# Performance work log

Hardware: AMD Instinct MI355X
Metric: run time of the kernel (lower is better)

## Reference

```python
import jax, jax.numpy as jnp
import numpy as np

B, S, D, H = 32, 512, 512, 8  # note: source requires S == D due to swapped shape tuple in multi_head_attention
DK = D // H  # 64
FF = 200     # hard-coded FFN width in source
LN_EPS = 1e-5


def setup_inputs() -> dict:
    key = jax.random.key(0)
    ks = jax.random.split(key, 20)
    s = 0.02
    return {
        "x": jax.random.normal(ks[0], (B, S, D), dtype=jnp.float32),
        # per-head projections, stacked: torch Linear weight shape is [out, in] = [DK, D]
        "Wq": jax.random.normal(ks[1], (H, DK, D), dtype=jnp.float32) * s,
        "bq": jax.random.normal(ks[2], (H, DK), dtype=jnp.float32) * s,
        "Wk": jax.random.normal(ks[3], (H, DK, D), dtype=jnp.float32) * s,
        "bk": jax.random.normal(ks[4], (H, DK), dtype=jnp.float32) * s,
        "Wv": jax.random.normal(ks[5], (H, DK, D), dtype=jnp.float32) * s,
        "bv": jax.random.normal(ks[6], (H, DK), dtype=jnp.float32) * s,
        "Wo": jax.random.normal(ks[7], (D, D), dtype=jnp.float32) * s,
        "bo": jax.random.normal(ks[8], (D,), dtype=jnp.float32) * s,
        "W1": jax.random.normal(ks[9], (FF, D), dtype=jnp.float32) * s,
        "b1": jax.random.normal(ks[10], (FF,), dtype=jnp.float32) * s,
        "W2": jax.random.normal(ks[11], (FF, FF), dtype=jnp.float32) * s,
        "b2": jax.random.normal(ks[12], (FF,), dtype=jnp.float32) * s,
        "W3": jax.random.normal(ks[13], (D, FF), dtype=jnp.float32) * s,
        "b3": jax.random.normal(ks[14], (D,), dtype=jnp.float32) * s,
        # single SHARED LayerNorm over last two dims (S, D)
        "gamma": jnp.ones((S, D), dtype=jnp.float32),
        "beta": jnp.zeros((S, D), dtype=jnp.float32),
    }


def _layernorm2d(y, gamma, beta):
    # torch LayerNorm(normalized_shape=(S, D)): normalize over last two axes, biased variance
    m = jnp.mean(y, axis=(-2, -1), keepdims=True)
    v = jnp.mean(jnp.square(y - m), axis=(-2, -1), keepdims=True)
    return (y - m) * jax.lax.rsqrt(v + LN_EPS) * gamma + beta


def reference(x, Wq, bq, Wk, bk, Wv, bv, Wo, bo, W1, b1, W2, b2, W3, b3, gamma, beta):
    # --- multi-head attention (vectorized over the original per-head Python loop) ---
    q = jnp.einsum('bsd,hkd->bhsk', x, Wq) + bq[None, :, None, :]
    k = jnp.einsum('bsd,hkd->bhsk', x, Wk) + bk[None, :, None, :]
    v = jnp.einsum('bsd,hkd->bhsk', x, Wv) + bv[None, :, None, :]
    scores = jnp.einsum('bhsk,bhtk->bhst', q, k) / jnp.sqrt(jnp.float32(DK))
    attn = jax.nn.softmax(scores, axis=-1)
    heads = jnp.einsum('bhst,bhtk->bhsk', attn, v)          # [B,H,S,DK]
    concat = heads.transpose(0, 2, 1, 3).reshape(B, S, D)    # concat heads along feature dim
    y = jnp.einsum('bsd,ed->bse', concat, Wo) + bo + x       # output proj + residual
    # --- post-attention LayerNorm (shared params) ---
    y = _layernorm2d(y, gamma, beta)
    # --- feed-forward: D -> 200 -> 200 -> D, residual, LayerNorm (same shared LN) ---
    f = jax.nn.relu(jnp.einsum('bsd,fd->bsf', y, W1) + b1)
    f = jax.nn.relu(jnp.einsum('bsf,gf->bsg', f, W2) + b2)
    f = jnp.einsum('bsf,df->bsd', f, W3) + b3
    y = _layernorm2d(f + y, gamma, beta)
    # --- final LayerNorm (same shared LN again) ---
    return _layernorm2d(y, gamma, beta)
```

## Files before the change

### kernel.cpp

```cpp
#include <hip/hip_runtime.h>
#include <hip/hip_bf16.h>
#include <stdint.h>

#define B_  32
#define S_  512
#define D_  512
#define H_  8
#define DK_ 64
#define FF_ 200
#define FFP 256
#define M_  (B_*S_)
#define MSD ((size_t)B_*S_*D_)
#define NQKV 1536

typedef __hip_bfloat16 bf16;
typedef __attribute__((ext_vector_type(8))) short short8;
typedef __attribute__((ext_vector_type(4))) float f32x4;
typedef __attribute__((ext_vector_type(4))) unsigned short us4;

__device__ inline float b2f(bf16 v) { return __bfloat162float(v); }
__device__ inline bf16  f2b(float v){ return __float2bfloat16(v); }
__device__ inline unsigned short f2bu(float v) {
  union { bf16 h; unsigned short u; } cv; cv.h = __float2bfloat16(v); return cv.u;
}
__device__ inline float bu2f(unsigned short u) {
  union { unsigned short u; bf16 h; } cv; cv.u = u; return b2f(cv.h);
}
__device__ __forceinline__ void async16(const bf16* g, bf16* l) {
  __builtin_amdgcn_global_load_lds((const __attribute__((address_space(1))) void*)g,
                                   (__attribute__((address_space(3))) void*)l, 16, 0, 0);
}

__global__ void detect_kernel(const unsigned short* __restrict__ xu, int* __restrict__ flag,
                              float* __restrict__ stats) {
  __shared__ int mx[256];
  const int tid = threadIdx.x;
  if (tid < 192) stats[tid] = 0.f;
  int m = 0;
  for (int i = tid * 2; i < 8192; i += 512) {
    int e = (xu[i] >> 7) & 0xFF;
    m = m > e ? m : e;
  }
  mx[tid] = m;
  __syncthreads();
  for (int st = 128; st; st >>= 1) {
    if (tid < st) mx[tid] = mx[tid] > mx[tid + st] ? mx[tid] : mx[tid + st];
    __syncthreads();
  }
  if (tid == 0) *flag = (mx[0] >= 0xC0) ? 1 : 0;
}

__global__ __launch_bounds__(256) void cvt_x8(const void* __restrict__ in, bf16* __restrict__ out,
                                              const int* __restrict__ flag) {
  const bool f32in = (*flag != 0);
  size_t i = ((size_t)blockIdx.x * 256 + threadIdx.x) * 8;
  const size_t stride = (size_t)gridDim.x * 256 * 8;
  for (; i < MSD; i += stride) {
    if (f32in) {
      const float4 a = ((const float4*)in)[i/4];
      const float4 b = ((const float4*)in)[i/4 + 1];
      uint4 o; unsigned short* po = (unsigned short*)&o;
      po[0]=f2bu(a.x); po[1]=f2bu(a.y); po[2]=f2bu(a.z); po[3]=f2bu(a.w);
      po[4]=f2bu(b.x); po[5]=f2bu(b.y); po[6]=f2bu(b.z); po[7]=f2bu(b.w);
      *(uint4*)((unsigned short*)out + i) = o;
    } else {
      *(uint4*)((unsigned short*)out + i) = *(const uint4*)((const unsigned short*)in + i);
    }
  }
}

struct Seg { const void* src; void* dst; int srcRows, srcK, dstK, total; };
struct Segs { Seg s[16]; unsigned int isbf; };

__global__ __launch_bounds__(256) void cvt_all(Segs sg, const int* __restrict__ flag) {
  const bool f32in = (*flag != 0);
  const int seg = blockIdx.x & 15;
  const Seg sd = sg.s[seg];
  const int stride = (gridDim.x >> 4) * 256;
  const bool nopad = (sd.srcK == sd.dstK);
  for (int i = (blockIdx.x >> 4) * 256 + threadIdx.x; i < sd.total; i += stride) {
    int sidx; bool valid;
    if (nopad) { sidx = i; valid = (i < sd.srcRows * sd.srcK); }
    else {
      int r = i / sd.dstK, c = i - r * sd.dstK;
      valid = (r < sd.srcRows) && (c < sd.srcK);
      sidx = r * sd.srcK + c;
    }
    float v = 0.f;
    if (valid) v = f32in ? ((const float*)sd.src)[sidx] : b2f(((const bf16*)sd.src)[sidx]);
    if (sg.isbf & (1u << seg)) ((unsigned short*)sd.dst)[i] = f2bu(v);
    else                       ((float*)sd.dst)[i] = v;
  }
}

template<int MODE, int STATS>
__global__ __launch_bounds__(256) void gemm_mfma(
    const bf16* __restrict__ A, const bf16* __restrict__ W, const float* __restrict__ bias,
    const bf16* __restrict__ R, bf16* __restrict__ C, int M, int N, int K,
    float* __restrict__ stats)
{
  __shared__ __align__(16) char smem[32768];
  bf16*  As  = (bf16*)smem;
  bf16*  Bs  = (bf16*)smem + 8192;
  float* Lf  = (float*)smem;
  float* red = (float*)(smem + 20480);

  const int tid  = threadIdx.x;
  const int bm   = blockIdx.x * 128;
  const int bn   = blockIdx.y * 128;
  const int w    = tid >> 6;
  const int lane = tid & 63;
  const int qd   = lane >> 4;
  const int ln   = lane & 15;
  const int wr   = (w >> 1) * 64;
  const int wc   = (w & 1) * 64;

  const bf16* srcA[4]; const bf16* srcB[4];
  bf16* dstA[4]; bf16* dstB[4];
#pragma unroll
  for (int i2 = 0; i2 < 4; i2++) {
    const int g   = w*4 + i2;
    const int row = (g & 7)*16 + (lane >> 2);
    const int col = (g >> 3)*32 + (lane & 3)*8;
    srcA[i2] = A + (size_t)(bm + row) * K + col;
    srcB[i2] = W + (size_t)(bn + row) * K + col;
    dstA[i2] = As + g*512 + lane*8;
    dstB[i2] = Bs + g*512 + lane*8;
  }

  f32x4 acc[4][4] = {};

  for (int k0 = 0; k0 < K; k0 += 64) {
#pragma unroll
    for (int i2 = 0; i2 < 4; i2++) {
      async16(srcA[i2] + k0, dstA[i2]);
      async16(srcB[i2] + k0, dstB[i2]);
    }
    __syncthreads();
#pragma unroll
    for (int kk = 0; kk < 2; kk++) {
      short8 af[4], bfr[4];
#pragma unroll
      for (int i = 0; i < 4; i++) af[i]  = *(const short8*)(As + kk*4096 + (wr + i*16 + ln)*32 + qd*8);
#pragma unroll
      for (int j = 0; j < 4; j++) bfr[j] = *(const short8*)(Bs + kk*4096 + (wc + j*16 + ln)*32 + qd*8);
#pragma unroll
      for (int i = 0; i < 4; i++)
#pragma unroll
        for (int j = 0; j < 4; j++)
          acc[i][j] = __builtin_amdgcn_mfma_f32_16x16x32_bf16(af[i], bfr[j], acc[i][j], 0, 0, 0);
    }
    __syncthreads();
  }

  float s_acc = 0.f, ss_acc = 0.f;
  const int lrbase = (w >> 1)*16 + qd*4;
#pragma unroll
  for (int i = 0; i < 4; i++) {
#pragma unroll
    for (int j = 0; j < 4; j++) {
      const int col = wc + j*16 + ln;
#pragma unroll
      for (int rg = 0; rg < 4; rg++)
        Lf[(lrbase + rg)*132 + col] = acc[i][j][rg];
    }
    __syncthreads();
#pragma unroll
    for (int pz = 0; pz < 2; pz++) {
      const int q   = tid + pz*256;
      const int r   = q >> 4;
      const int nof = (q & 15)*8;
      const int m   = bm + (r >> 4)*64 + i*16 + (r & 15);
      const int n   = bn + nof;
      f32x4 v0 = *(const f32x4*)(Lf + r*132 + nof);
      f32x4 v1 = *(const f32x4*)(Lf + r*132 + nof + 4);
      f32x4 b0 = *(const f32x4*)(bias + n);
      f32x4 b1 = *(const f32x4*)(bias + n + 4);
      float vals[8];
#pragma unroll
      for (int e = 0; e < 4; e++) { vals[e] = v0[e] + b0[e]; vals[4+e] = v1[e] + b1[e]; }
      if (MODE == 1) {
#pragma unroll
        for (int e = 0; e < 8; e++) vals[e] = fmaxf(vals[e], 0.f);
      }
      if (MODE == 2) {
        const uint4 rv = *(const uint4*)((const unsigned short*)R + (size_t)m * N + n);
        const unsigned short* rp = (const unsigned short*)&rv;
#pragma unroll
        for (int e = 0; e < 8; e++) vals[e] += bu2f(rp[e]);
      }
      if (STATS) {
#pragma unroll
        for (int e = 0; e < 8; e++) { s_acc += vals[e]; ss_acc += vals[e]*vals[e]; }
      }
      uint4 o; unsigned short* op = (unsigned short*)&o;
#pragma unroll
      for (int e = 0; e < 8; e++) op[e] = f2bu(vals[e]);
      *(uint4*)((unsigned short*)C + (size_t)m * N + n) = o;
    }
    __syncthreads();
  }

  if (STATS) {
    red[tid] = s_acc; red[256 + tid] = ss_acc;
    __syncthreads();
    for (int st = 128; st; st >>= 1) {
      if (tid < st) { red[tid] += red[tid + st]; red[256 + tid] += red[256 + tid + st]; }
      __syncthreads();
    }
    if (tid == 0) {
      const int b = bm >> 9;
      atomicAdd(&stats[b*2],     red[0]);
      atomicAdd(&stats[b*2 + 1], red[256]);
    }
  }
}

__global__ __launch_bounds__(1024, 4) void attn_lds(const bf16* __restrict__ qkv,
                                                    bf16* __restrict__ cat)
{
  __shared__ bf16 Ks[2 * 512 * 32];
  __shared__ bf16 Vs[64 * 520];
  __shared__ bf16 pbuf[16][16][40];

  const int tid  = threadIdx.x;
  const int w    = tid >> 6;
  const int lane = tid & 63;
  const int qd   = lane >> 4;
  const int ln   = lane & 15;
  const int bh   = blockIdx.x;
  const int b    = bh >> 3, h = bh & 7;
  const bf16* base = qkv + (size_t)b * 512 * NQKV + h * 64;

  for (int c = tid; c < 4096; c += 1024) {
    int part = c & 3, key = (c >> 2) & 511, ks = c >> 11;
    async16(base + (size_t)key * NQKV + 512 + ks*32 + part*8, Ks + c*8);
  }
  for (int c = tid; c < 4096; c += 1024) {
    int dkg = c & 7, key = c >> 3;
    uint4 vv = *(const uint4*)(base + (size_t)key * NQKV + 1024 + dkg*8);
    const unsigned short* pv = (const unsigned short*)&vv;
#pragma unroll
    for (int j = 0; j < 8; j++)
      *(unsigned short*)&Vs[(dkg*8 + j)*520 + key] = pv[j];
  }
  short8 bq[2][2];
#pragma unroll
  for (int qt = 0; qt < 2; qt++)
#pragma unroll
    for (int ks = 0; ks < 2; ks++)
      bq[qt][ks] = *(const short8*)(base + (size_t)(w*32 + qt*16 + ln) * NQKV + ks*32 + qd*8);

  __syncthreads();

  bf16 (*pb)[40] = pbuf[w];
  f32x4 o[2][4] = {};
  float l[2] = {0.f, 0.f};

  for (int st = 0; st < 16; st++) {
    short8 ak[2][2];
#pragma unroll
    for (int kt = 0; kt < 2; kt++)
#pragma unroll
      for (int ks = 0; ks < 2; ks++)
        ak[kt][ks] = *(const short8*)(Ks + ks*16384 + (st*32 + kt*16 + ln)*32 + qd*8);
    f32x4 s[2][2] = {};
#pragma unroll
    for (int kt = 0; kt < 2; kt++)
#pragma unroll
      for (int qt = 0; qt < 2; qt++) {
        s[kt][qt] = __builtin_amdgcn_mfma_f32_16x16x32_bf16(ak[kt][0], bq[qt][0], s[kt][qt], 0, 0, 0);
        s[kt][qt] = __builtin_amdgcn_mfma_f32_16x16x32_bf16(ak[kt][1], bq[qt][1], s[kt][qt], 0, 0, 0);
      }
    float e[2][2][4];
#pragma unroll
    for (int kt = 0; kt < 2; kt++)
#pragma unroll
      for (int qt = 0; qt < 2; qt++)
#pragma unroll
        for (int rg = 0; rg < 4; rg++) {
          float ev = __expf(s[kt][qt][rg] * 0.125f);
          e[kt][qt][rg] = ev;
          l[qt] += ev;
        }
#pragma unroll
    for (int qt = 0; qt < 2; qt++) {
#pragma unroll
      for (int kt = 0; kt < 2; kt++) {
        uint2 pk;
        pk.x = (unsigned)f2bu(e[kt][qt][0]) | ((unsigned)f2bu(e[kt][qt][1]) << 16);
        pk.y = (unsigned)f2bu(e[kt][qt][2]) | ((unsigned)f2bu(e[kt][qt][3]) << 16);
        *(uint2*)&pb[ln][kt*16 + qd*4] = pk;
      }
      short8 ap = *(const short8*)&pb[ln][qd*8];
#pragma unroll
      for (int nt = 0; nt < 4; nt++) {
        short8 bv = *(const short8*)(Vs + (nt*16 + ln)*520 + st*32 + qd*8);
        o[qt][nt] = __builtin_amdgcn_mfma_f32_16x16x32_bf16(ap, bv, o[qt][nt], 0, 0, 0);
      }
    }
  }

#pragma unroll
  for (int qt = 0; qt < 2; qt++) {
    l[qt] += __shfl_xor(l[qt], 16);
    l[qt] += __shfl_xor(l[qt], 32);
  }
  float inv0 = 1.f / l[0], inv1 = 1.f / l[1];

  const size_t crow0 = (size_t)(b*S_ + w*32) * D_ + h*DK_;
#pragma unroll
  for (int qt = 0; qt < 2; qt++) {
#pragma unroll
    for (int rg = 0; rg < 4; rg++) {
      float ivv = __shfl(qt ? inv1 : inv0, qd*4 + rg);
      int r = qt*16 + qd*4 + rg;
      bf16* cp = cat + crow0 + (size_t)r * D_ + ln;
#pragma unroll
      for (int nt = 0; nt < 4; nt++) cp[nt*16] = f2b(o[qt][nt][rg] * ivv);
    }
  }
}

__global__ __launch_bounds__(256) void ln_b16_b16(const bf16* __restrict__ in,
    const float* __restrict__ stats, const float* __restrict__ gamma,
    const float* __restrict__ beta, bf16* __restrict__ out)
{
  const int b = blockIdx.x >> 4;
  const float invN = 1.f / (float)(S_*D_);
  const float m    = stats[b*2] * invN;
  const float var  = stats[b*2+1] * invN - m*m;
  const float rstd = rsqrtf(var + 1e-5f);
  size_t v = (size_t)b * 65536 + (blockIdx.x & 15) * 4096 + threadIdx.x;
#pragma unroll 4
  for (int it = 0; it < 16; it++, v += 256) {
    us4 xi = *(const us4*)((const unsigned short*)in + v*4);
    size_t e = (v * 4) & (S_*D_ - 1);
    float4 g = *(const float4*)(gamma + e);
    float4 bt= *(const float4*)(beta + e);
    us4 o;
    o[0] = f2bu((bu2f(xi[0]) - m) * rstd * g.x + bt.x);
    o[1] = f2bu((bu2f(xi[1]) - m) * rstd * g.y + bt.y);
    o[2] = f2bu((bu2f(xi[2]) - m) * rstd * g.z + bt.z);
    o[3] = f2bu((bu2f(xi[3]) - m) * rstd * g.w + bt.w);
    *(us4*)((unsigned short*)out + v*4) = o;
  }
}

__global__ __launch_bounds__(256) void ln_b16_b16_stats(const bf16* __restrict__ in,
    const float* __restrict__ stats, const float* __restrict__ gamma,
    const float* __restrict__ beta, bf16* __restrict__ out, float* __restrict__ stats3)
{
  __shared__ float red[512];
  const int b = blockIdx.x >> 4;
  const float invN = 1.f / (float)(S_*D_);
  const float m    = stats[b*2] * invN;
  const float var  = stats[b*2+1] * invN - m*m;
  const float rstd = rsqrtf(var + 1e-5f);
  size_t v = (size_t)b * 65536 + (blockIdx.x & 15) * 4096 + threadIdx.x;
  float s_acc = 0.f, ss_acc = 0.f;
#pragma unroll 4
  for (int it = 0; it < 16; it++, v += 256) {
    us4 xi = *(const us4*)((const unsigned short*)in + v*4);
    size_t e = (v * 4) & (S_*D_ - 1);
    float4 g = *(const float4*)(gamma + e);
    float4 bt= *(const float4*)(beta + e);
    float o0 = (bu2f(xi[0]) - m) * rstd * g.x + bt.x;
    float o1 = (bu2f(xi[1]) - m) * rstd * g.y + bt.y;
    float o2 = (bu2f(xi[2]) - m) * rstd * g.z + bt.z;
    float o3 = (bu2f(xi[3]) - m) * rstd * g.w + bt.w;
    us4 o;
    o[0] = f2bu(o0); o[1] = f2bu(o1); o[2] = f2bu(o2); o[3] = f2bu(o3);
    s_acc  += o0 + o1 + o2 + o3;
    ss_acc += o0*o0 + o1*o1 + o2*o2 + o3*o3;
    *(us4*)((unsigned short*)out + v*4) = o;
  }
  const int tid = threadIdx.x;
  red[tid] = s_acc; red[256 + tid] = ss_acc;
  __syncthreads();
  for (int st = 128; st; st >>= 1) {
    if (tid < st) { red[tid] += red[tid + st]; red[256 + tid] += red[256 + tid + st]; }
    __syncthreads();
  }
  if (tid == 0) {
    atomicAdd(&stats3[b*2],     red[0]);
    atomicAdd(&stats3[b*2 + 1], red[256]);
  }
}

__global__ __launch_bounds__(256) void ln_apply_out(const bf16* __restrict__ in,
    const float* __restrict__ stats, const float* __restrict__ gamma,
    const float* __restrict__ beta, void* __restrict__ out, const int* __restrict__ flag)
{
  const bool f32 = (*flag != 0);
  const int b = blockIdx.x >> 4;
  const float invN = 1.f / (float)(S_*D_);
  const float m    = stats[b*2] * invN;
  const float var  = stats[b*2+1] * invN - m*m;
  const float rstd = rsqrtf(var + 1e-5f);
  size_t v = (size_t)b * 65536 + (blockIdx.x & 15) * 4096 + threadIdx.x;
#pragma unroll 4
  for (int it = 0; it < 16; it++, v += 256) {
    us4 xi = *(const us4*)((const unsigned short*)in + v*4);
    size_t e = (v * 4) & (S_*D_ - 1);
    float4 g = *(const float4*)(gamma + e);
    float4 bt= *(const float4*)(beta + e);
    float4 o;
    o.x = (bu2f(xi[0]) - m) * rstd * g.x + bt.x;
    o.y = (bu2f(xi[1]) - m) * rstd * g.y + bt.y;
    o.z = (bu2f(xi[2]) - m) * rstd * g.z + bt.z;
    o.w = (bu2f(xi[3]) - m) * rstd * g.w + bt.w;
    if (f32) ((float4*)out)[v] = o;
    else {
      us4 ob;
      ob[0] = f2bu(o.x); ob[1] = f2bu(o.y); ob[2] = f2bu(o.z); ob[3] = f2bu(o.w);
      *(us4*)((unsigned short*)out + v*4) = ob;
    }
  }
}

extern "C" void kernel_launch(void* const* d_in, const int* in_sizes, int n_in,
                              void* d_out, int out_size, void* d_ws, size_t ws_size,
                              hipStream_t stream)
{
  char* p = (char*)d_ws;
  auto alloc_b = [&](size_t elems) { void* r = p; p += elems * 2; return (bf16*)r; };
  auto alloc_f = [&](size_t elems) {
    p = (char*)(((uintptr_t)p + 15) & ~(uintptr_t)15); void* r = p; p += elems * 4; return (float*)r;
  };

  bf16* xb   = alloc_b(MSD);
  bf16* qkv  = alloc_b(3 * MSD);
  bf16* catb = alloc_b(MSD);
  bf16* wqkv = alloc_b(3 * 512 * 512);
  bf16* wo   = alloc_b(512 * 512);
  bf16* w1p  = alloc_b((size_t)FFP * 512);
  bf16* w2p  = alloc_b((size_t)FFP * FFP);
  bf16* w3p  = alloc_b((size_t)512 * FFP);
  float* bqkv= alloc_f(3 * 512);
  float* bo  = alloc_f(512);
  float* b1p = alloc_f(FFP);
  float* b2p = alloc_f(FFP);
  float* b3  = alloc_f(512);
  float* gm  = alloc_f((size_t)S_ * D_);
  float* bt  = alloc_f((size_t)S_ * D_);
  float* stats = alloc_f(192);
  int*   flag  = (int*)alloc_f(16);
  if ((size_t)(p - (char*)d_ws) > ws_size) return;

  bf16* y1b = qkv;
  bf16* f1  = qkv + MSD;
  bf16* f2  = qkv + MSD + (size_t)M_ * FFP;
  bf16* yA  = qkv + 2 * MSD;
  bf16* yB  = catb;
  bf16* y2b = yA;
  float* st1 = stats, *st2 = stats + 64, *st3 = stats + 128;

  detect_kernel<<<1, 256, 0, stream>>>((const unsigned short*)d_in[0], flag, stats);
  cvt_x8<<<2048, 256, 0, stream>>>(d_in[0], xb, flag);

  Segs sg;
  sg.s[0]  = { d_in[1],  wqkv,               512, 512, 512, 512*512 };
  sg.s[1]  = { d_in[3],  wqkv + 512*512,     512, 512, 512, 512*512 };
  sg.s[2]  = { d_in[5],  wqkv + 2*512*512,   512, 512, 512, 512*512 };
  sg.s[3]  = { d_in[7],  wo,                 512, 512, 512, 512*512 };
  sg.s[4]  = { d_in[9],  w1p,                FF_, 512, 512, FFP*512 };
  sg.s[5]  = { d_in[11], w2p,                FF_, FF_, FFP, FFP*FFP };
  sg.s[6]  = { d_in[13], w3p,                512, FF_, FFP, 512*FFP };
  sg.s[7]  = { d_in[2],  bqkv,               1, 512, 512, 512 };
  sg.s[8]  = { d_in[4],  bqkv + 512,         1, 512, 512, 512 };
  sg.s[9]  = { d_in[6],  bqkv + 1024,        1, 512, 512, 512 };
  sg.s[10] = { d_in[8],  bo,                 1, 512, 512, 512 };
  sg.s[11] = { d_in[10], b1p,                1, FF_, FFP, FFP };
  sg.s[12] = { d_in[12], b2p,                1, FF_, FFP, FFP };
  sg.s[13] = { d_in[14], b3,                 1, 512, 512, 512 };
  sg.s[14] = { d_in[15], gm,                 1, S_*D_, S_*D_, S_*D_ };
  sg.s[15] = { d_in[16], bt,                 1, S_*D_, S_*D_, S_*D_ };
  sg.isbf = 0x007F;
  cvt_all<<<1024, 256, 0, stream>>>(sg, flag);

  dim3 blk(256);

  gemm_mfma<0, 0><<<dim3(M_/128, NQKV/128), blk, 0, stream>>>(
      xb, wqkv, bqkv, nullptr, qkv, M_, NQKV, 512, nullptr);

  attn_lds<<<B_*H_, 1024, 0, stream>>>(qkv, catb);

  gemm_mfma<2, 1><<<dim3(M_/128, 4), blk, 0, stream>>>(
      catb, wo, bo, xb, yA, M_, 512, 512, st1);

  ln_b16_b16<<<512, blk, 0, stream>>>(yA, st1, gm, bt, y1b);

  gemm_mfma<1, 0><<<dim3(M_/128, 2), blk, 0, stream>>>(
      y1b, w1p, b1p, nullptr, f1, M_, FFP, 512, nullptr);
  gemm_mfma<1, 0><<<dim3(M_/128, 2), blk, 0, stream>>>(
      f1, w2p, b2p, nullptr, f2, M_, FFP, FFP, nullptr);
  gemm_mfma<2, 1><<<dim3(M_/128, 4), blk, 0, stream>>>(
      f2, w3p, b3, y1b, yB, M_, 512, FFP, st2);

  ln_b16_b16_stats<<<512, blk, 0, stream>>>(yB, st2, gm, bt, y2b, st3);
  ln_apply_out<<<512, blk, 0, stream>>>(y2b, st3, gm, bt, d_out, flag);
}
```

Baseline: 294.5 us.

## Shrink GEMM K-tile to 32, store LN gamma/beta as bf16, interleave LN blocks

The GEMM main loop now stages a 32-wide K slice per iteration instead of 64, cutting shared memory from 32KB to about 18.5KB so more blocks can be resident, at the cost of twice as many barriers per K. LayerNorm gamma and beta are converted to bf16 once, halving their read traffic in the three LN kernels. LN block indexing is changed so consecutive blocks walk different batches while sharing the same gamma/beta slice, which should improve cache reuse. The bf16 gamma/beta adds a small rounding error.

```diff
diff --git a/kernel.cpp b/kernel.cpp
--- a/kernel.cpp
+++ b/kernel.cpp
@@ -99,11 +99,11 @@
     const bf16* __restrict__ R, bf16* __restrict__ C, int M, int N, int K,
     float* __restrict__ stats)
 {
-  __shared__ __align__(16) char smem[32768];
+  __shared__ __align__(16) char smem[18944];
   bf16*  As  = (bf16*)smem;
-  bf16*  Bs  = (bf16*)smem + 8192;
+  bf16*  Bs  = (bf16*)(smem + 8192);
   float* Lf  = (float*)smem;
-  float* red = (float*)(smem + 20480);
+  float* red = (float*)(smem + 16896);
 
   const int tid  = threadIdx.x;
   const int bm   = blockIdx.x * 128;
@@ -115,41 +115,36 @@
   const int wr   = (w >> 1) * 64;
   const int wc   = (w & 1) * 64;
 
-  const bf16* srcA[4]; const bf16* srcB[4];
-  bf16* dstA[4]; bf16* dstB[4];
-#pragma unroll
-  for (int i2 = 0; i2 < 4; i2++) {
-    const int g   = w*4 + i2;
-    const int row = (g & 7)*16 + (lane >> 2);
-    const int col = (g >> 3)*32 + (lane & 3)*8;
-    srcA[i2] = A + (size_t)(bm + row) * K + col;
-    srcB[i2] = W + (size_t)(bn + row) * K + col;
-    dstA[i2] = As + g*512 + lane*8;
-    dstB[i2] = Bs + g*512 + lane*8;
-  }
+  const int r0 = lane >> 2;
+  const int ch = (lane & 3) * 8;
+  const bf16* Ag0 = A + (size_t)(bm + w*16 + r0) * K + ch;
+  const bf16* Ag1 = Ag0 + (size_t)64 * K;
+  const bf16* Bg0 = W + (size_t)(bn + w*16 + r0) * K + ch;
+  const bf16* Bg1 = Bg0 + (size_t)64 * K;
+  bf16* Al0 = As + w*512 + lane*8;
+  bf16* Al1 = Al0 + 2048;
+  bf16* Bl0 = Bs + w*512 + lane*8;
+  bf16* Bl1 = Bl0 + 2048;
 
   f32x4 acc[4][4] = {};
 
-  for (int k0 = 0; k0 < K; k0 += 64) {
-#pragma unroll
-    for (int i2 = 0; i2 < 4; i2++) {
-      async16(srcA[i2] + k0, dstA[i2]);
-      async16(srcB[i2] + k0, dstB[i2]);
-    }
-    __syncthreads();
-#pragma unroll
-    for (int kk = 0; kk < 2; kk++) {
-      short8 af[4], bfr[4];
-#pragma unroll
-      for (int i = 0; i < 4; i++) af[i]  = *(const short8*)(As + kk*4096 + (wr + i*16 + ln)*32 + qd*8);
-#pragma unroll
-      for (int j = 0; j < 4; j++) bfr[j] = *(const short8*)(Bs + kk*4096 + (wc + j*16 + ln)*32 + qd*8);
-#pragma unroll
-      for (int i = 0; i < 4; i++)
-#pragma unroll
-        for (int j = 0; j < 4; j++)
-          acc[i][j] = __builtin_amdgcn_mfma_f32_16x16x32_bf16(af[i], bfr[j], acc[i][j], 0, 0, 0);
-    }
+  for (int k0 = 0; k0 < K; k0 += 32) {
+    async16(Ag0 + k0, Al0);
+    async16(Ag1 + k0, Al1);
+    async16(Bg0 + k0, Bl0);
+    async16(Bg1 + k0, Bl1);
+    __syncthreads();
+
+    short8 af[4], bfr[4];
+#pragma unroll
+    for (int i = 0; i < 4; i++) af[i]  = *(const short8*)(As + (wr + i*16 + ln)*32 + qd*8);
+#pragma unroll
+    for (int j = 0; j < 4; j++) bfr[j] = *(const short8*)(Bs + (wc + j*16 + ln)*32 + qd*8);
+#pragma unroll
+    for (int i = 0; i < 4; i++)
+#pragma unroll
+      for (int j = 0; j < 4; j++)
+        acc[i][j] = __builtin_amdgcn_mfma_f32_16x16x32_bf16(af[i], bfr[j], acc[i][j], 0, 0, 0);
     __syncthreads();
   }
 
@@ -323,52 +318,54 @@
 }
 
 __global__ __launch_bounds__(256) void ln_b16_b16(const bf16* __restrict__ in,
-    const float* __restrict__ stats, const float* __restrict__ gamma,
-    const float* __restrict__ beta, bf16* __restrict__ out)
+    const float* __restrict__ stats, const bf16* __restrict__ gamma,
+    const bf16* __restrict__ beta, bf16* __restrict__ out)
 {
-  const int b = blockIdx.x >> 4;
+  const int b     = blockIdx.x & 31;
+  const int slice = blockIdx.x >> 5;
   const float invN = 1.f / (float)(S_*D_);
   const float m    = stats[b*2] * invN;
   const float var  = stats[b*2+1] * invN - m*m;
   const float rstd = rsqrtf(var + 1e-5f);
-  size_t v = (size_t)b * 65536 + (blockIdx.x & 15) * 4096 + threadIdx.x;
+  size_t v = (size_t)b * 65536 + slice * 4096 + threadIdx.x;
 #pragma unroll 4
   for (int it = 0; it < 16; it++, v += 256) {
     us4 xi = *(const us4*)((const unsigned short*)in + v*4);
     size_t e = (v * 4) & (S_*D_ - 1);
-    float4 g = *(const float4*)(gamma + e);
-    float4 bt= *(const float4*)(beta + e);
+    us4 g4 = *(const us4*)((const unsigned short*)gamma + e);
+    us4 b4 = *(const us4*)((const unsigned short*)beta + e);
     us4 o;
-    o[0] = f2bu((bu2f(xi[0]) - m) * rstd * g.x + bt.x);
-    o[1] = f2bu((bu2f(xi[1]) - m) * rstd * g.y + bt.y);
-    o[2] = f2bu((bu2f(xi[2]) - m) * rstd * g.z + bt.z);
-    o[3] = f2bu((bu2f(xi[3]) - m) * rstd * g.w + bt.w);
+    o[0] = f2bu((bu2f(xi[0]) - m) * rstd * bu2f(g4[0]) + bu2f(b4[0]));
+    o[1] = f2bu((bu2f(xi[1]) - m) * rstd * bu2f(g4[1]) + bu2f(b4[1]));
+    o[2] = f2bu((bu2f(xi[2]) - m) * rstd * bu2f(g4[2]) + bu2f(b4[2]));
+    o[3] = f2bu((bu2f(xi[3]) - m) * rstd * bu2f(g4[3]) + bu2f(b4[3]));
     *(us4*)((unsigned short*)out + v*4) = o;
   }
 }
 
 __global__ __launch_bounds__(256) void ln_b16_b16_stats(const bf16* __restrict__ in,
-    const float* __restrict__ stats, const float* __restrict__ gamma,
-    const float* __restrict__ beta, bf16* __restrict__ out, float* __restrict__ stats3)
+    const float* __restrict__ stats, const bf16* __restrict__ gamma,
+    const bf16* __restrict__ beta, bf16* __restrict__ out, float* __restrict__ stats3)
 {
   __shared__ float red[512];
-  const int b = blockIdx.x >> 4;
+  const int b     = blockIdx.x & 31;
+  const int slice = blockIdx.x >> 5;
   const float invN = 1.f / (float)(S_*D_);
   const float m    = stats[b*2] * invN;
   const float var  = stats[b*2+1] * invN - m*m;
   const float rstd = rsqrtf(var + 1e-5f);
-  size_t v = (size_t)b * 65536 + (blockIdx.x & 15) * 4096 + threadIdx.x;
+  size_t v = (size_t)b * 65536 + slice * 4096 + threadIdx.x;
   float s_acc = 0.f, ss_acc = 0.f;
 #pragma unroll 4
   for (int it = 0; it < 16; it++, v += 256) {
     us4 xi = *(const us4*)((const unsigned short*)in + v*4);
     size_t e = (v * 4) & (S_*D_ - 1);
-    float4 g = *(const float4*)(gamma + e);
-    float4 bt= *(const float4*)(beta + e);
-    float o0 = (bu2f(xi[0]) - m) * rstd * g.x + bt.x;
-    float o1 = (bu2f(xi[1]) - m) * rstd * g.y + bt.y;
-    float o2 = (bu2f(xi[2]) - m) * rstd * g.z + bt.z;
-    float o3 = (bu2f(xi[3]) - m) * rstd * g.w + bt.w;
+    us4 g4 = *(const us4*)((const unsigned short*)gamma + e);
+    us4 b4 = *(const us4*)((const unsigned short*)beta + e);
+    float o0 = (bu2f(xi[0]) - m) * rstd * bu2f(g4[0]) + bu2f(b4[0]);
+    float o1 = (bu2f(xi[1]) - m) * rstd * bu2f(g4[1]) + bu2f(b4[1]);
+    float o2 = (bu2f(xi[2]) - m) * rstd * bu2f(g4[2]) + bu2f(b4[2]);
+    float o3 = (bu2f(xi[3]) - m) * rstd * bu2f(g4[3]) + bu2f(b4[3]);
     us4 o;
     o[0] = f2bu(o0); o[1] = f2bu(o1); o[2] = f2bu(o2); o[3] = f2bu(o3);
     s_acc  += o0 + o1 + o2 + o3;
@@ -389,27 +386,28 @@
 }
 
 __global__ __launch_bounds__(256) void ln_apply_out(const bf16* __restrict__ in,
-    const float* __restrict__ stats, const float* __restrict__ gamma,
-    const float* __restrict__ beta, void* __restrict__ out, const int* __restrict__ flag)
+    const float* __restrict__ stats, const bf16* __restrict__ gamma,
+    const bf16* __restrict__ beta, void* __restrict__ out, const int* __restrict__ flag)
 {
   const bool f32 = (*flag != 0);
-  const int b = blockIdx.x >> 4;
+  const int b     = blockIdx.x & 31;
+  const int slice = blockIdx.x >> 5;
   const float invN = 1.f / (float)(S_*D_);
   const float m    = stats[b*2] * invN;
   const float var  = stats[b*2+1] * invN - m*m;
   const float rstd = rsqrtf(var + 1e-5f);
-  size_t v = (size_t)b * 65536 + (blockIdx.x & 15) * 4096 + threadIdx.x;
+  size_t v = (size_t)b * 65536 + slice * 4096 + threadIdx.x;
 #pragma unroll 4
   for (int it = 0; it < 16; it++, v += 256) {
     us4 xi = *(const us4*)((const unsigned short*)in + v*4);
     size_t e = (v * 4) & (S_*D_ - 1);
-    float4 g = *(const float4*)(gamma + e);
-    float4 bt= *(const float4*)(beta + e);
+    us4 g4 = *(const us4*)((const unsigned short*)gamma + e);
+    us4 b4 = *(const us4*)((const unsigned short*)beta + e);
     float4 o;
-    o.x = (bu2f(xi[0]) - m) * rstd * g.x + bt.x;
-    o.y = (bu2f(xi[1]) - m) * rstd * g.y + bt.y;
-    o.z = (bu2f(xi[2]) - m) * rstd * g.z + bt.z;
-    o.w = (bu2f(xi[3]) - m) * rstd * g.w + bt.w;
+    o.x = (bu2f(xi[0]) - m) * rstd * bu2f(g4[0]) + bu2f(b4[0]);
+    o.y = (bu2f(xi[1]) - m) * rstd * bu2f(g4[1]) + bu2f(b4[1]);
+    o.z = (bu2f(xi[2]) - m) * rstd * bu2f(g4[2]) + bu2f(b4[2]);
+    o.w = (bu2f(xi[3]) - m) * rstd * bu2f(g4[3]) + bu2f(b4[3]);
     if (f32) ((float4*)out)[v] = o;
     else {
       us4 ob;
@@ -437,13 +435,13 @@
   bf16* w1p  = alloc_b((size_t)FFP * 512);
   bf16* w2p  = alloc_b((size_t)FFP * FFP);
   bf16* w3p  = alloc_b((size_t)512 * FFP);
+  bf16* gm   = alloc_b((size_t)S_ * D_);
+  bf16* bt   = alloc_b((size_t)S_ * D_);
   float* bqkv= alloc_f(3 * 512);
   float* bo  = alloc_f(512);
   float* b1p = alloc_f(FFP);
   float* b2p = alloc_f(FFP);
   float* b3  = alloc_f(512);
-  float* gm  = alloc_f((size_t)S_ * D_);
-  float* bt  = alloc_f((size_t)S_ * D_);
   float* stats = alloc_f(192);
   int*   flag  = (int*)alloc_f(16);
   if ((size_t)(p - (char*)d_ws) > ws_size) return;
@@ -476,7 +474,7 @@
   sg.s[13] = { d_in[14], b3,                 1, 512, 512, 512 };
   sg.s[14] = { d_in[15], gm,                 1, S_*D_, S_*D_, S_*D_ };
   sg.s[15] = { d_in[16], bt,                 1, S_*D_, S_*D_, S_*D_ };
-  sg.isbf = 0x007F;
+  sg.isbf = 0xC07F;
   cvt_all<<<1024, 256, 0, stream>>>(sg, flag);
 
   dim3 blk(256);
```

Measured after the change: 301.6 us. 2.4% more time.
